# Kernel tuning notes

Hardware: AMD Instinct MI355X
Metric: run time of the kernel (lower is better)

The kernel has to match this reference:

```python
import jax, jax.numpy as jnp
import numpy as np

H = 512   # hidden_size
V = 5000  # output_size (vocab)
B = 128   # batch
S = 64    # encoder source length
T = 52    # max_trajectory_length


def setup_inputs() -> dict:
    key = jax.random.key(0)
    ks = jax.random.split(key, 16)
    sc = 0.05
    rn = lambda k, shape: jax.random.normal(k, shape, dtype=jnp.float32) * sc
    return dict(
        encoder_outputs=jax.random.normal(ks[0], (B, S, H), dtype=jnp.float32),
        h0=jax.random.normal(ks[1], (1, B, H), dtype=jnp.float32),
        c0=jax.random.normal(ks[2], (1, B, H), dtype=jnp.float32),
        target_tensor=jax.random.randint(ks[3], (B, T), 0, V),
        emb=rn(ks[4], (V, H)),
        Wa=rn(ks[5], (H, H)), ba=jnp.zeros((H,), jnp.float32),
        Ua=rn(ks[6], (H, H)), bu=jnp.zeros((H,), jnp.float32),
        Va=rn(ks[7], (H,)), bv=jnp.zeros((), jnp.float32),
        W_ih=rn(ks[8], (4 * H, 2 * H)), W_hh=rn(ks[9], (4 * H, H)),
        b_ih=jnp.zeros((4 * H,), jnp.float32), b_hh=jnp.zeros((4 * H,), jnp.float32),
        Wout=rn(ks[10], (V, H)), bout=jnp.zeros((V,), jnp.float32),
    )


def reference(encoder_outputs, h0, c0, target_tensor, emb,
              Wa, ba, Ua, bu, Va, bv,
              W_ih, W_hh, b_ih, b_hh, Wout, bout):
    # Dropout is identity in eval mode.
    b = target_tensor.shape[0]
    # Ua(keys) is constant across decode steps -> precompute once. [B,S,H]
    keys_proj = jnp.einsum('bsh,kh->bsk', encoder_outputs, Ua) + bu
    # Teacher forcing: input at step i is target[:, i-1], step 0 is token 0.
    tokens = jnp.concatenate(
        [jnp.zeros((b, 1), target_tensor.dtype), target_tensor[:, :-1]], axis=1)  # [B,T]

    def step(carry, tok):
        h, c = carry                                # [B,H] each
        x = emb[tok]                                # embedding lookup [B,H]
        q = h @ Wa.T + ba                           # Wa(query) [B,H]
        scores = jnp.tanh(q[:, None, :] + keys_proj) @ Va + bv  # [B,S]
        w = jax.nn.softmax(scores, axis=-1)         # attn weights [B,S]
        ctx = jnp.einsum('bs,bsh->bh', w, encoder_outputs)       # context [B,H]
        xi = jnp.concatenate([x, ctx], axis=-1)     # [B,2H]
        gates = xi @ W_ih.T + b_ih + h @ W_hh.T + b_hh           # [B,4H]
        i_g, f_g, g_g, o_g = jnp.split(gates, 4, axis=-1)        # torch gate order i,f,g,o
        c = jax.nn.sigmoid(f_g) * c + jax.nn.sigmoid(i_g) * jnp.tanh(g_g)
        h = jax.nn.sigmoid(o_g) * jnp.tanh(c)
        logits = h @ Wout.T + bout                  # [B,V]
        return (h, c), (logits, w)

    (h, c), (logits, attn) = jax.lax.scan(step, (h0[0], c0[0]), tokens.T)
    logits = jnp.transpose(logits, (1, 0, 2))       # [B,T,V]
    log_probs = jax.nn.log_softmax(logits, axis=-1)
    attn = jnp.transpose(attn, (1, 0, 2))           # [B,T,S]
    return log_probs, (h[None], c[None]), attn
```

## Files before the change

kernel.cpp:

```cpp
#include <hip/hip_runtime.h>
#include <math.h>

#define H 512
#define V 5000
#define BB 128
#define SS 64
#define TT 52
#define NB 160

typedef __attribute__((ext_vector_type(8))) short bf16x8;
typedef __attribute__((ext_vector_type(4))) float f32x4;
typedef __attribute__((ext_vector_type(2))) float f32x2;

__device__ __forceinline__ unsigned short f2b(float f) {
    unsigned u = __float_as_uint(f);
    return (unsigned short)((u + 0x7fffu + ((u >> 16) & 1u)) >> 16);
}
__device__ __forceinline__ float b2f(unsigned short u) {
    return __uint_as_float((unsigned)u << 16);
}
__device__ __forceinline__ float ftanh(float x) {
    return 1.f - 2.f / (1.f + __expf(2.f * x));
}
__device__ __forceinline__ float fsig(float x) {
    return 1.f / (1.f + __expf(-x));
}
__device__ __forceinline__ unsigned char f2fp8(float f) {
    return (unsigned char)__builtin_amdgcn_cvt_pk_fp8_f32(f, f, 0, 0);
}

#define CLD16_BODY \
        "global_load_dwordx4 %0, %16, off sc0 sc1\n\t"              \
        "global_load_dwordx4 %1, %16, off offset:64 sc0 sc1\n\t"    \
        "global_load_dwordx4 %2, %16, off offset:128 sc0 sc1\n\t"   \
        "global_load_dwordx4 %3, %16, off offset:192 sc0 sc1\n\t"   \
        "global_load_dwordx4 %4, %16, off offset:256 sc0 sc1\n\t"   \
        "global_load_dwordx4 %5, %16, off offset:320 sc0 sc1\n\t"   \
        "global_load_dwordx4 %6, %16, off offset:384 sc0 sc1\n\t"   \
        "global_load_dwordx4 %7, %16, off offset:448 sc0 sc1\n\t"   \
        "global_load_dwordx4 %8, %16, off offset:512 sc0 sc1\n\t"   \
        "global_load_dwordx4 %9, %16, off offset:576 sc0 sc1\n\t"   \
        "global_load_dwordx4 %10, %16, off offset:640 sc0 sc1\n\t"  \
        "global_load_dwordx4 %11, %16, off offset:704 sc0 sc1\n\t"  \
        "global_load_dwordx4 %12, %16, off offset:768 sc0 sc1\n\t"  \
        "global_load_dwordx4 %13, %16, off offset:832 sc0 sc1\n\t"  \
        "global_load_dwordx4 %14, %16, off offset:896 sc0 sc1\n\t"  \
        "global_load_dwordx4 %15, %16, off offset:960 sc0 sc1"
#define CLD16_OUTS(r) \
          "=v"(r[0]), "=v"(r[1]), "=v"(r[2]), "=v"(r[3]),   \
          "=v"(r[4]), "=v"(r[5]), "=v"(r[6]), "=v"(r[7]),   \
          "=v"(r[8]), "=v"(r[9]), "=v"(r[10]), "=v"(r[11]), \
          "=v"(r[12]), "=v"(r[13]), "=v"(r[14]), "=v"(r[15])

__device__ __forceinline__ void cld_row16_nw(const unsigned short* p, bf16x8* r)
{
    asm volatile(CLD16_BODY : CLD16_OUTS(r) : "v"(p) : "memory");
}
__device__ __forceinline__ void cld_row16(const unsigned short* p, bf16x8* r)
{
    asm volatile(CLD16_BODY "\n\ts_waitcnt vmcnt(0)"
                 : CLD16_OUTS(r) : "v"(p) : "memory");
}
__device__ __forceinline__ void cld_f_2(const float* p0, const float* p1,
                                        float& a, float& b)
{
    asm volatile(
        "global_load_dword %0, %2, off sc0 sc1\n\t"
        "global_load_dword %1, %3, off sc0 sc1\n\t"
        "s_waitcnt vmcnt(0)"
        : "=v"(a), "=v"(b) : "v"(p0), "v"(p1) : "memory");
}
__device__ __forceinline__ void cld_f4p(const float* p, f32x4& a, f32x4& b)
{
    asm volatile(
        "global_load_dwordx4 %0, %2, off sc0 sc1\n\t"
        "global_load_dwordx4 %1, %2, off offset:16 sc0 sc1\n\t"
        "s_waitcnt vmcnt(0)"
        : "=v"(a), "=v"(b) : "v"(p) : "memory");
}
__device__ __forceinline__ void cst_f(float* p, float v)
{
    asm volatile("global_store_dword %0, %1, off sc0 sc1"
                 :: "v"(p), "v"(v) : "memory");
}
__device__ __forceinline__ void cst_u32(unsigned* p, unsigned v)
{
    asm volatile("global_store_dword %0, %1, off sc0 sc1"
                 :: "v"(p), "v"(v) : "memory");
}
__device__ __forceinline__ void cst_h(unsigned short* p, unsigned short v)
{
    unsigned vv = v;
    asm volatile("global_store_short %0, %1, off sc0 sc1"
                 :: "v"(p), "v"(vv) : "memory");
}

__global__ __launch_bounds__(256)
void prep_w(const float* __restrict__ Wa, const float* __restrict__ Whh,
            const float* __restrict__ Wih,
            const float* __restrict__ ba, const float* __restrict__ bih,
            const float* __restrict__ bhh,
            const float* __restrict__ Ua, const float* __restrict__ Wout,
            const float* __restrict__ enc,
            unsigned short* __restrict__ Wbig, unsigned short* __restrict__ Wc,
            unsigned short* __restrict__ Uab, unsigned short* __restrict__ Woutb,
            unsigned short* __restrict__ encb, float* __restrict__ bbig)
{
    const int stride = gridDim.x * blockDim.x;
    const int t0 = blockIdx.x * blockDim.x + threadIdx.x;
    for (int idx = t0; idx < 2560 * 1024; idx += stride) {
        const int j = idx >> 10, k = idx & 1023;
        float v;
        if (j < H) v = (k < H) ? Wa[j * H + k] : 0.f;
        else { const int n = j - H; v = (k < H) ? Whh[n * H + k] : Wih[n * 2 * H + (k - H)]; }
        Wbig[idx] = f2b(v);
    }
    for (int idx = t0; idx < 2048 * 512; idx += stride) {
        const int n = idx >> 9, k = idx & 511;
        Wc[idx] = f2b(Wih[n * 2 * H + H + k]);
    }
    for (int idx = t0; idx < 512 * 512; idx += stride)   Uab[idx]   = f2b(Ua[idx]);
    for (int idx = t0; idx < V * 512; idx += stride)     Woutb[idx] = f2b(Wout[idx]);
    for (int idx = t0; idx < BB * SS * H; idx += stride) encb[idx]  = f2b(enc[idx]);
    for (int j = t0; j < 2560; j += stride)
        bbig[j] = (j < H) ? ba[j] : bih[j - H] + bhh[j - H];
}

__global__ __launch_bounds__(256)
void gather_x(const float* __restrict__ emb, const int* __restrict__ tgt,
              unsigned short* __restrict__ xall)
{
    const int stride = gridDim.x * blockDim.x;
    for (int idx = blockIdx.x * blockDim.x + threadIdx.x; idx < TT * BB * H; idx += stride) {
        const int k = idx & 511;
        const int row = idx >> 9;
        const int t = row >> 7, b = row & 127;
        const int tok = (t == 0) ? 0 : tgt[b * TT + t - 1];
        xall[idx] = f2b(emb[(size_t)tok * H + k]);
    }
}

template<int OUT_MODE, int PERMUTE>
__global__ __launch_bounds__(256, 2)
void gemm_mfma(const unsigned short* __restrict__ A,
               const unsigned short* __restrict__ B,
               const float* __restrict__ bias,
               float* __restrict__ Cf, unsigned short* __restrict__ Cb,
               unsigned char* __restrict__ C8,
               int M, int N)
{
    __shared__ unsigned short As[128][72];
    __shared__ unsigned short Bs[128][72];
    const int tid = threadIdx.x;
    const int m0 = blockIdx.y * 128, n0 = blockIdx.x * 128;
    const int lane = tid & 63, wv = tid >> 6;
    const int qm = (wv >> 1) * 64, qn = (wv & 1) * 64;
    const int fr = lane & 15, fg = lane >> 4;
    f32x4 acc[4][4];
#pragma unroll
    for (int i = 0; i < 4; ++i)
#pragma unroll
        for (int j = 0; j < 4; ++j) acc[i][j] = (f32x4){0.f, 0.f, 0.f, 0.f};

    const int srow = tid >> 3, sc = (tid & 7) * 8;
    for (int k0 = 0; k0 < H; k0 += 64) {
#pragma unroll
        for (int u = 0; u < 4; ++u) {
            const int row = srow + u * 32;
            *(uint4*)&As[row][sc] = *(const uint4*)&A[(size_t)(m0 + row) * H + k0 + sc];
            int nr = n0 + row; if (nr > N - 1) nr = N - 1;
            *(uint4*)&Bs[row][sc] = *(const uint4*)&B[(size_t)nr * H + k0 + sc];
        }
        __syncthreads();
#pragma unroll
        for (int ks = 0; ks < 2; ++ks) {
            const int kk = ks * 32 + fg * 8;
            bf16x8 av[4], bv[4];
#pragma unroll
            for (int i = 0; i < 4; ++i) {
                av[i] = *(const bf16x8*)&As[qm + i * 16 + fr][kk];
                bv[i] = *(const bf16x8*)&Bs[qn + i * 16 + fr][kk];
            }
#pragma unroll
            for (int i = 0; i < 4; ++i)
#pragma unroll
                for (int j = 0; j < 4; ++j)
                    acc[i][j] = __builtin_amdgcn_mfma_f32_16x16x32_bf16(av[i], bv[j], acc[i][j], 0, 0, 0);
        }
        __syncthreads();
    }
#pragma unroll
    for (int i = 0; i < 4; ++i) {
        const int r0 = m0 + qm + i * 16 + fg * 4;
#pragma unroll
        for (int j = 0; j < 4; ++j) {
            const int col = n0 + qn + j * 16 + fr;
            if (col < N) {
                const float bi = bias ? bias[col] : 0.f;
#pragma unroll
                for (int v = 0; v < 4; ++v) {
                    const int r = r0 + v;
                    const float val = acc[i][j][v] + bi;
                    if (OUT_MODE == 1) {
                        Cb[(size_t)r * N + col] = f2b(val);
                    } else if (OUT_MODE == 2) {
                        C8[(size_t)r * N + col] = f2fp8(val);
                    } else {
                        const size_t orow = PERMUTE ? ((size_t)(r & (BB - 1)) * TT + (r >> 7))
                                                    : (size_t)r;
                        Cf[orow * (size_t)N + col] = val;
                    }
                }
            }
        }
    }
}

__device__ __forceinline__ void signal_flag(unsigned* flags, unsigned step)
{
    __syncthreads();
    if (threadIdx.x == 0)
        __hip_atomic_store(&flags[blockIdx.x * 32], step, __ATOMIC_RELAXED,
                           __HIP_MEMORY_SCOPE_AGENT);
}
__device__ __forceinline__ void wait_flags(unsigned* flags, int lo, int hi,
                                           unsigned step)
{
    for (int i = lo + (int)threadIdx.x; i < hi; i += 256) {
        while (__hip_atomic_load(&flags[i * 32], __ATOMIC_RELAXED,
                                 __HIP_MEMORY_SCOPE_AGENT) < step)
            __builtin_amdgcn_s_sleep(1);
    }
    __syncthreads();
}
__device__ __forceinline__ void wait_flags_wave32(unsigned* flags, int lo,
                                                  unsigned step)
{
    const int lane = threadIdx.x & 63;
    if (lane < 32) {
        while (__hip_atomic_load(&flags[(lo + lane) * 32], __ATOMIC_RELAXED,
                                 __HIP_MEMORY_SCOPE_AGENT) < step)
            __builtin_amdgcn_s_sleep(1);
    }
}

struct PParams {
    const float* h0;
    const float* c0;
    const unsigned short* keysb;
    const unsigned char* encW8;
    const float* Va;
    const float* bv;
    const float* bbig;
    const unsigned short* Wbig;
    const unsigned short* xall;
    unsigned short* hbf;
    float* Y;
    unsigned short* hallb;
    float* attn;
    float* out_h;
    float* out_c;
    unsigned* flags;
};

__global__ __launch_bounds__(256, 1)
void persist(PParams p)
{
    __shared__ unsigned short WA[16][1032];
    __shared__ float qa_s[H];
    __shared__ float va_s[H];
    __shared__ float part[SS][4];
    __shared__ float wbuf[SS];
    __shared__ float gbuf[4 * H];
    __shared__ float cs[H];

    const int tid  = threadIdx.x;
    const int beta = blockIdx.x;
    const int j0   = (beta < 128) ? (512 + beta * 16) : ((beta - 128) * 16);

    for (int i = beta * 256 + tid; i < BB * H; i += NB * 256)
        cst_h(&p.hbf[i], f2b(p.h0[i]));
    for (int idx = tid; idx < 16 * 128; idx += 256) {
        const int r = idx >> 7, ch = idx & 127;
        *(uint4*)&WA[r][ch * 8] = *(const uint4*)&p.Wbig[(size_t)(j0 + r) * 1024 + ch * 8];
    }
    if (beta < 128) {
        for (int j = tid; j < H; j += 256) cs[j] = p.c0[beta * H + j];
        for (int i = tid; i < H; i += 256) va_s[i] = p.Va[i];
    }
    signal_flag(p.flags, 1);
    wait_flags(p.flags, 0, NB, 1);

    for (int t = 0; t < TT; ++t) {
        const unsigned sp1 = 2 * t + 2;
        const unsigned sh  = 2 * t + 3;
        {
            const int wv = tid >> 6, lane = tid & 63;
            const int r = lane & 15, g = lane >> 4;
            const int b0 = wv * 32, b1 = b0 + 16;
            const int ko = g * 8;
            wait_flags_wave32(p.flags, b0, sp1 - 1);
            bf16x8 hr0[16], hr1[16];
            cld_row16_nw(p.hbf + (size_t)(b0 + r) * H + ko, hr0);
            cld_row16  (p.hbf + (size_t)(b1 + r) * H + ko, hr1);
            __builtin_amdgcn_sched_barrier(0);
            f32x4 acc0 = {0.f, 0.f, 0.f, 0.f};
            f32x4 acc1 = {0.f, 0.f, 0.f, 0.f};
#pragma unroll
            for (int ks = 0; ks < 16; ++ks) {
                bf16x8 bf = *(const bf16x8*)&WA[r][ks * 32 + ko];
                acc0 = __builtin_amdgcn_mfma_f32_16x16x32_bf16(hr0[ks], bf, acc0, 0, 0, 0);
                acc1 = __builtin_amdgcn_mfma_f32_16x16x32_bf16(hr1[ks], bf, acc1, 0, 0, 0);
            }
            const unsigned short* x0p = p.xall + ((size_t)t * BB + b0 + r) * H + ko;
            const unsigned short* x1p = p.xall + ((size_t)t * BB + b1 + r) * H + ko;
#pragma unroll
            for (int ks = 0; ks < 16; ++ks) {
                bf16x8 bf = *(const bf16x8*)&WA[r][512 + ks * 32 + ko];
                acc0 = __builtin_amdgcn_mfma_f32_16x16x32_bf16(*(const bf16x8*)&x0p[ks * 32], bf, acc0, 0, 0, 0);
                acc1 = __builtin_amdgcn_mfma_f32_16x16x32_bf16(*(const bf16x8*)&x1p[ks * 32], bf, acc1, 0, 0, 0);
            }
            const float bb = p.bbig[j0 + r];
#pragma unroll
            for (int i = 0; i < 4; ++i) {
                cst_f(p.Y + (size_t)(b0 + g * 4 + i) * 2560 + j0 + r, acc0[i] + bb);
                cst_f(p.Y + (size_t)(b1 + g * 4 + i) * 2560 + j0 + r, acc1[i] + bb);
            }
        }
        signal_flag(p.flags, sp1);

        if (beta < 128) {
            const int b = beta;
            const float* yrow = p.Y + (size_t)b * 2560;
            wait_flags(p.flags, 128, NB, sp1);
            cld_f_2(yrow + tid, yrow + 256 + tid, qa_s[tid], qa_s[tid + 256]);
            __syncthreads();
            const int s = tid >> 2, q = tid & 3;
            const unsigned short* kp = p.keysb + ((size_t)b * SS + s) * H + q * 128;
            const float* qp = qa_s + q * 128;
            const float* vp = va_s + q * 128;
            float a2 = 0.f, a2b = 0.f;
#pragma unroll 4
            for (int i = 0; i < 128; i += 2) {
                a2  += ftanh(qp[i] + b2f(kp[i])) * vp[i];
                a2b += ftanh(qp[i + 1] + b2f(kp[i + 1])) * vp[i + 1];
            }
            part[s][q] = a2 + a2b;
            __syncthreads();
            if (tid < 64) {
                float sc = part[tid][0] + part[tid][1] + part[tid][2] + part[tid][3] + p.bv[0];
                float m = sc;
                for (int o = 32; o; o >>= 1) m = fmaxf(m, __shfl_xor(m, o));
                const float e = __expf(sc - m);
                float ss = e;
                for (int o = 32; o; o >>= 1) ss += __shfl_xor(ss, o);
                const float w = e / ss;
                wbuf[tid] = w;
                p.attn[((size_t)b * TT + t) * SS + tid] = w;
            }
            wait_flags(p.flags, 0, 128, sp1);
            {
                float gc[8] = {0.f, 0.f, 0.f, 0.f, 0.f, 0.f, 0.f, 0.f};
                const unsigned char* ew = p.encW8 + (size_t)b * SS * 2048 + tid * 8;
#pragma unroll 8
                for (int s2 = 0; s2 < SS; ++s2) {
                    const float w2 = wbuf[s2];
                    const uint2 u = *(const uint2*)(ew + (size_t)s2 * 2048);
                    const f32x2 e01 = __builtin_amdgcn_cvt_pk_f32_fp8(u.x, 0);
                    const f32x2 e23 = __builtin_amdgcn_cvt_pk_f32_fp8(u.x, 1);
                    const f32x2 e45 = __builtin_amdgcn_cvt_pk_f32_fp8(u.y, 0);
                    const f32x2 e67 = __builtin_amdgcn_cvt_pk_f32_fp8(u.y, 1);
                    gc[0] += w2 * e01[0]; gc[1] += w2 * e01[1];
                    gc[2] += w2 * e23[0]; gc[3] += w2 * e23[1];
                    gc[4] += w2 * e45[0]; gc[5] += w2 * e45[1];
                    gc[6] += w2 * e67[0]; gc[7] += w2 * e67[1];
                }
                f32x4 y0, y1;
                cld_f4p(yrow + 512 + tid * 8, y0, y1);
#pragma unroll
                for (int i = 0; i < 4; ++i) {
                    gbuf[tid * 8 + i]     = gc[i] + y0[i];
                    gbuf[tid * 8 + 4 + i] = gc[4 + i] + y1[i];
                }
            }
            __syncthreads();
            {
                const int last = (t == TT - 1);
                unsigned hpack = 0;
                float hn2[2], cn2[2];
#pragma unroll
                for (int u = 0; u < 2; ++u) {
                    const int j = tid * 2 + u;
                    const float ig = gbuf[j];
                    const float fg = gbuf[512 + j];
                    const float gg = gbuf[1024 + j];
                    const float og = gbuf[1536 + j];
                    const float co = cs[j];
                    const float cn = fsig(fg) * co + fsig(ig) * ftanh(gg);
                    const float hn = fsig(og) * ftanh(cn);
                    cs[j] = cn;
                    hn2[u] = hn; cn2[u] = cn;
                    hpack |= ((unsigned)f2b(hn)) << (16 * u);
                }
                cst_u32((unsigned*)&p.hbf[b * H + tid * 2], hpack);
                *(unsigned*)&p.hallb[((size_t)t * BB + b) * H + tid * 2] = hpack;
                if (last) {
#pragma unroll
                    for (int u = 0; u < 2; ++u) {
                        p.out_h[b * H + tid * 2 + u] = hn2[u];
                        p.out_c[b * H + tid * 2 + u] = cn2[u];
                    }
                }
            }
            signal_flag(p.flags, sh);
        }
    }
}

__global__ __launch_bounds__(256)
void logsoftmax_rows(float* __restrict__ P)
{
    __shared__ float red[256];
    float* p = P + (size_t)blockIdx.x * V;
    const int tid = threadIdx.x;
    float m = -1e30f;
    for (int i = tid; i < V; i += 256) m = fmaxf(m, p[i]);
    red[tid] = m; __syncthreads();
    for (int sft = 128; sft; sft >>= 1) {
        if (tid < sft) red[tid] = fmaxf(red[tid], red[tid + sft]);
        __syncthreads();
    }
    m = red[0]; __syncthreads();
    float ssum = 0.f;
    for (int i = tid; i < V; i += 256) ssum += __expf(p[i] - m);
    red[tid] = ssum; __syncthreads();
    for (int sft = 128; sft; sft >>= 1) {
        if (tid < sft) red[tid] += red[tid + sft];
        __syncthreads();
    }
    const float lse = m + __logf(red[0]);
    for (int i = tid; i < V; i += 256) p[i] -= lse;
}

extern "C" void kernel_launch(void* const* d_in, const int* in_sizes, int n_in,
                              void* d_out, int out_size, void* d_ws, size_t ws_size,
                              hipStream_t stream)
{
    (void)in_sizes; (void)n_in; (void)out_size; (void)ws_size;
    const float* enc  = (const float*)d_in[0];
    const float* h0   = (const float*)d_in[1];
    const float* c0   = (const float*)d_in[2];
    const int*   tgt  = (const int*)  d_in[3];
    const float* emb  = (const float*)d_in[4];
    const float* Wa   = (const float*)d_in[5];
    const float* ba   = (const float*)d_in[6];
    const float* Ua   = (const float*)d_in[7];
    const float* bu   = (const float*)d_in[8];
    const float* Va   = (const float*)d_in[9];
    const float* bv   = (const float*)d_in[10];
    const float* Wih  = (const float*)d_in[11];
    const float* Whh  = (const float*)d_in[12];
    const float* bih  = (const float*)d_in[13];
    const float* bhh  = (const float*)d_in[14];
    const float* Wout = (const float*)d_in[15];
    const float* bout = (const float*)d_in[16];

    float* ws = (float*)d_ws;
    float* Y    = ws;
    float* bbig = Y + 327680;
    unsigned* flags = (unsigned*)(bbig + 2560);
    unsigned short* Wbig  = (unsigned short*)(flags + 5504);
    unsigned short* Wc    = Wbig + 2621440;
    unsigned short* Uab   = Wc + 1048576;
    unsigned short* Woutb = Uab + 262144;
    unsigned short* encb  = Woutb + 2560000;
    unsigned short* keysb = encb + 4194304;
    unsigned short* xall  = keysb + 4194304;
    unsigned short* hallb = xall + 3407872;
    unsigned short* hbf   = hallb + 3407872;
    unsigned char*  encW8 = (unsigned char*)(hbf + 65536);

    float* out    = (float*)d_out;
    float* out_h  = out + (size_t)BB * TT * V;
    float* out_c  = out_h + BB * H;
    float* out_at = out_c + BB * H;

    hipMemsetAsync(flags, 0, 5504 * sizeof(unsigned), stream);

    prep_w<<<dim3(2048), dim3(256), 0, stream>>>(
        Wa, Whh, Wih, ba, bih, bhh, Ua, Wout, enc, Wbig, Wc, Uab, Woutb, encb, bbig);
    gather_x<<<dim3(512), dim3(256), 0, stream>>>(emb, tgt, xall);

    gemm_mfma<1, 0><<<dim3(4, 64), dim3(256), 0, stream>>>(
        encb, Uab, bu, nullptr, keysb, nullptr, BB * SS, H);
    gemm_mfma<2, 0><<<dim3(16, 64), dim3(256), 0, stream>>>(
        encb, Wc, nullptr, nullptr, nullptr, encW8, BB * SS, 2048);

    PParams pp;
    pp.h0 = h0; pp.c0 = c0; pp.keysb = keysb; pp.encW8 = encW8;
    pp.Va = Va; pp.bv = bv; pp.bbig = bbig;
    pp.Wbig = Wbig; pp.xall = xall;
    pp.hbf = hbf; pp.Y = Y; pp.hallb = hallb;
    pp.attn = out_at; pp.out_h = out_h; pp.out_c = out_c;
    pp.flags = flags;
    persist<<<dim3(NB), dim3(256), 0, stream>>>(pp);

    gemm_mfma<0, 1><<<dim3(40, 52), dim3(256), 0, stream>>>(
        hallb, Woutb, bout, out, nullptr, nullptr, TT * BB, V);
    logsoftmax_rows<<<dim3(BB * TT), dim3(256), 0, stream>>>(out);
}
```

Measured before the change: 1.444 ms.

## Split sync flags by phase and replicate them to reduce polling contention

Replaces the single per-block flag array with separate flag arrays for the qa, gate and h phases, each written in 8 replicas so that each block polls its own replica (selected by blockIdx & 7). This is meant to cut contention on shared cache lines and remove the double-step counter. Attention key loads are also vectorised into 8-wide bf16 loads. It costs more flag memory, a larger memset and extra atomic stores per block per step.

```diff
diff --git a/kernel.cpp b/kernel.cpp
--- a/kernel.cpp
+++ b/kernel.cpp
@@ -216,32 +216,13 @@
     }
 }
 
-__device__ __forceinline__ void signal_flag(unsigned* flags, unsigned step)
-{
-    __syncthreads();
-    if (threadIdx.x == 0)
-        __hip_atomic_store(&flags[blockIdx.x * 32], step, __ATOMIC_RELAXED,
-                           __HIP_MEMORY_SCOPE_AGENT);
-}
-__device__ __forceinline__ void wait_flags(unsigned* flags, int lo, int hi,
-                                           unsigned step)
-{
-    for (int i = lo + (int)threadIdx.x; i < hi; i += 256) {
-        while (__hip_atomic_load(&flags[i * 32], __ATOMIC_RELAXED,
-                                 __HIP_MEMORY_SCOPE_AGENT) < step)
-            __builtin_amdgcn_s_sleep(1);
-    }
-    __syncthreads();
-}
-__device__ __forceinline__ void wait_flags_wave32(unsigned* flags, int lo,
-                                                  unsigned step)
-{
-    const int lane = threadIdx.x & 63;
-    if (lane < 32) {
-        while (__hip_atomic_load(&flags[(lo + lane) * 32], __ATOMIC_RELAXED,
-                                 __HIP_MEMORY_SCOPE_AGENT) < step)
-            __builtin_amdgcn_s_sleep(1);
-    }
+__device__ __forceinline__ void poll_ge(unsigned* a, unsigned step)
+{
+    if (__hip_atomic_load(a, __ATOMIC_RELAXED, __HIP_MEMORY_SCOPE_AGENT) >= step)
+        return;
+    do {
+        __builtin_amdgcn_s_sleep(2);
+    } while (__hip_atomic_load(a, __ATOMIC_RELAXED, __HIP_MEMORY_SCOPE_AGENT) < step);
 }
 
 struct PParams {
@@ -260,7 +241,10 @@
     float* attn;
     float* out_h;
     float* out_c;
-    unsigned* flags;
+    unsigned* pflag;
+    unsigned* qaflag;
+    unsigned* gateflag;
+    unsigned* hflag;
 };
 
 __global__ __launch_bounds__(256, 1)
@@ -276,6 +260,7 @@
 
     const int tid  = threadIdx.x;
     const int beta = blockIdx.x;
+    const int rep  = beta & 7;
     const int j0   = (beta < 128) ? (512 + beta * 16) : ((beta - 128) * 16);
 
     for (int i = beta * 256 + tid; i < BB * H; i += NB * 256)
@@ -288,18 +273,22 @@
         for (int j = tid; j < H; j += 256) cs[j] = p.c0[beta * H + j];
         for (int i = tid; i < H; i += 256) va_s[i] = p.Va[i];
     }
-    signal_flag(p.flags, 1);
-    wait_flags(p.flags, 0, NB, 1);
+    __syncthreads();
+    if (tid == 0)
+        __hip_atomic_store(&p.pflag[beta * 32], 1u, __ATOMIC_RELAXED,
+                           __HIP_MEMORY_SCOPE_AGENT);
+    for (int i = tid; i < NB; i += 256) poll_ge(&p.pflag[i * 32], 1u);
+    __syncthreads();
 
     for (int t = 0; t < TT; ++t) {
-        const unsigned sp1 = 2 * t + 2;
-        const unsigned sh  = 2 * t + 3;
+        const unsigned st = (unsigned)(t + 1);
         {
             const int wv = tid >> 6, lane = tid & 63;
             const int r = lane & 15, g = lane >> 4;
             const int b0 = wv * 32, b1 = b0 + 16;
             const int ko = g * 8;
-            wait_flags_wave32(p.flags, b0, sp1 - 1);
+            if (t > 0 && lane < 32)
+                poll_ge(&p.hflag[(rep * 128 + b0 + lane) * 32], (unsigned)t);
             bf16x8 hr0[16], hr1[16];
             cld_row16_nw(p.hbf + (size_t)(b0 + r) * H + ko, hr0);
             cld_row16  (p.hbf + (size_t)(b1 + r) * H + ko, hr1);
@@ -327,12 +316,21 @@
                 cst_f(p.Y + (size_t)(b1 + g * 4 + i) * 2560 + j0 + r, acc1[i] + bb);
             }
         }
-        signal_flag(p.flags, sp1);
+        __syncthreads();
+        if (tid < 8) {
+            if (beta < 128)
+                __hip_atomic_store(&p.gateflag[(tid * 128 + beta) * 32], st,
+                                   __ATOMIC_RELAXED, __HIP_MEMORY_SCOPE_AGENT);
+            else
+                __hip_atomic_store(&p.qaflag[(tid * 32 + beta - 128) * 32], st,
+                                   __ATOMIC_RELAXED, __HIP_MEMORY_SCOPE_AGENT);
+        }
 
         if (beta < 128) {
             const int b = beta;
             const float* yrow = p.Y + (size_t)b * 2560;
-            wait_flags(p.flags, 128, NB, sp1);
+            if (tid < 32) poll_ge(&p.qaflag[(rep * 32 + tid) * 32], st);
+            __syncthreads();
             cld_f_2(yrow + tid, yrow + 256 + tid, qa_s[tid], qa_s[tid + 256]);
             __syncthreads();
             const int s = tid >> 2, q = tid & 3;
@@ -340,10 +338,15 @@
             const float* qp = qa_s + q * 128;
             const float* vp = va_s + q * 128;
             float a2 = 0.f, a2b = 0.f;
-#pragma unroll 4
-            for (int i = 0; i < 128; i += 2) {
-                a2  += ftanh(qp[i] + b2f(kp[i])) * vp[i];
-                a2b += ftanh(qp[i + 1] + b2f(kp[i + 1])) * vp[i + 1];
+#pragma unroll
+            for (int i8 = 0; i8 < 16; ++i8) {
+                bf16x8 kv = *(const bf16x8*)&kp[i8 * 8];
+#pragma unroll
+                for (int u = 0; u < 8; u += 2) {
+                    const int i = i8 * 8 + u;
+                    a2  += ftanh(qp[i]     + b2f((unsigned short)kv[u]))     * vp[i];
+                    a2b += ftanh(qp[i + 1] + b2f((unsigned short)kv[u + 1])) * vp[i + 1];
+                }
             }
             part[s][q] = a2 + a2b;
             __syncthreads();
@@ -358,7 +361,8 @@
                 wbuf[tid] = w;
                 p.attn[((size_t)b * TT + t) * SS + tid] = w;
             }
-            wait_flags(p.flags, 0, 128, sp1);
+            if (tid < 128) poll_ge(&p.gateflag[(rep * 128 + tid) * 32], st);
+            __syncthreads();
             {
                 float gc[8] = {0.f, 0.f, 0.f, 0.f, 0.f, 0.f, 0.f, 0.f};
                 const unsigned char* ew = p.encW8 + (size_t)b * SS * 2048 + tid * 8;
@@ -412,7 +416,10 @@
                     }
                 }
             }
-            signal_flag(p.flags, sh);
+            __syncthreads();
+            if (tid < 8)
+                __hip_atomic_store(&p.hflag[(tid * 128 + beta) * 32], st,
+                                   __ATOMIC_RELAXED, __HIP_MEMORY_SCOPE_AGENT);
         }
     }
 }
@@ -469,7 +476,11 @@
     float* Y    = ws;
     float* bbig = Y + 327680;
     unsigned* flags = (unsigned*)(bbig + 2560);
-    unsigned short* Wbig  = (unsigned short*)(flags + 5504);
+    unsigned* pflag    = flags;
+    unsigned* qaflag   = flags + 5120;
+    unsigned* gateflag = flags + 13312;
+    unsigned* hflag    = flags + 46080;
+    unsigned short* Wbig  = (unsigned short*)(flags + 78848);
     unsigned short* Wc    = Wbig + 2621440;
     unsigned short* Uab   = Wc + 1048576;
     unsigned short* Woutb = Uab + 262144;
@@ -485,7 +496,7 @@
     float* out_c  = out_h + BB * H;
     float* out_at = out_c + BB * H;
 
-    hipMemsetAsync(flags, 0, 5504 * sizeof(unsigned), stream);
+    hipMemsetAsync(flags, 0, 78848 * sizeof(unsigned), stream);
 
     prep_w<<<dim3(2048), dim3(256), 0, stream>>>(
         Wa, Whh, Wih, ba, bih, bhh, Ua, Wout, enc, Wbig, Wc, Uab, Woutb, encb, bbig);
@@ -502,7 +513,7 @@
     pp.Wbig = Wbig; pp.xall = xall;
     pp.hbf = hbf; pp.Y = Y; pp.hallb = hallb;
     pp.attn = out_at; pp.out_h = out_h; pp.out_c = out_c;
-    pp.flags = flags;
+    pp.pflag = pflag; pp.qaflag = qaflag; pp.gateflag = gateflag; pp.hflag = hflag;
     persist<<<dim3(NB), dim3(256), 0, stream>>>(pp);
 
     gemm_mfma<0, 1><<<dim3(40, 52), dim3(256), 0, stream>>>(
```

Measured after the change: 1.468 ms. About the same (+1.6%).
